# Optimization experiments

Measured on AMD Instinct MI355X. Metric: run time of the kernel, lower is better.

The kernel has to match this reference:

```python
import jax, jax.numpy as jnp
import numpy as np


def _conv2d(x, w, b, padding):
    # x: [N,C,H,W], w: [O,I,kh,kw]
    y = jax.lax.conv_general_dilated(
        x, w, window_strides=(1, 1), padding=padding,
        dimension_numbers=("NCHW", "OIHW", "NCHW"))
    return y + b[None, :, None, None]


def setup_inputs() -> dict:
    key = jax.random.key(0)
    ks = jax.random.split(key, 9)
    s = 0.05
    return {
        "x": jax.random.normal(ks[0], (16, 4, 512, 512), dtype=jnp.float32),
        "w1": jax.random.normal(ks[1], (32, 4, 3, 3), dtype=jnp.float32) * s,
        "b1": jax.random.normal(ks[2], (32,), dtype=jnp.float32) * s,
        "w2": jax.random.normal(ks[3], (4, 32, 3, 3), dtype=jnp.float32) * s,
        "b2": jax.random.normal(ks[4], (4,), dtype=jnp.float32) * s,
        "w_se1": jax.random.normal(ks[5], (16, 32, 1, 1), dtype=jnp.float32) * s,
        "b_se1": jax.random.normal(ks[6], (16,), dtype=jnp.float32) * s,
        "w_se2": jax.random.normal(ks[7], (32, 16, 1, 1), dtype=jnp.float32) * s,
        "b_se2": jax.random.normal(ks[8], (32,), dtype=jnp.float32) * s,
    }


def reference(x, w1, b1, w2, b2, w_se1, b_se1, w_se2, b_se2):
    x1 = x
    # module1: 3x3 conv (4->32) + ReLU
    h = jax.nn.relu(_conv2d(x, w1, b1, padding="SAME"))  # [N,32,H,W]
    se_in = h
    # SE branch: global avg pool -> 1x1 conv -> ReLU -> 1x1 conv -> sigmoid
    p = jnp.mean(h, axis=(2, 3), keepdims=True)  # [N,32,1,1]
    p = jax.nn.relu(_conv2d(p, w_se1, b_se1, padding="VALID"))  # [N,16,1,1]
    p = jax.nn.sigmoid(_conv2d(p, w_se2, b_se2, padding="VALID"))  # [N,32,1,1]
    h = p * se_in  # broadcast channel scaling
    # module2: 3x3 conv (32->4) + ReLU
    h = jax.nn.relu(_conv2d(h, w2, b2, padding="SAME"))  # [N,4,H,W]
    return h * x1  # residual multiply
```

## Files before the change

### kernel.cpp

```cpp
#include <hip/hip_runtime.h>
#include <math.h>

#define IMG 512

typedef __attribute__((ext_vector_type(4))) short short4_t;
typedef __attribute__((ext_vector_type(8))) short short8;
typedef __attribute__((ext_vector_type(4))) float f32x4;
typedef __attribute__((ext_vector_type(16))) float f32x16;
typedef __attribute__((ext_vector_type(2))) unsigned int u32x2;

__device__ __forceinline__ unsigned short f2bf(float f) {
  unsigned u = __builtin_bit_cast(unsigned, f);
  u += 0x7FFFu + ((u >> 16) & 1u);
  return (unsigned short)(u >> 16);
}
__device__ __forceinline__ unsigned cvtpk(float lo, float hi) {
  unsigned r;
  asm("v_cvt_pk_bf16_f32 %0, %1, %2" : "=v"(r) : "v"(lo), "v"(hi));
  return r;
}

__global__ __launch_bounds__(256) void k_prep(const float* __restrict__ w1,
                                              unsigned short* __restrict__ w1f) {
  const int t = threadIdx.x;
  if (t < 192) {
    const int kk = t >> 6, lane = t & 63;
    const int oc = lane & 31, hi = lane >> 5;
#pragma unroll
    for (int j = 0; j < 8; ++j) {
      const int dxp = 2 * hi + (j >> 2), ic = j & 3;
      float v = (dxp < 3) ? w1[((oc * 4 + ic) * 3 + kk) * 3 + dxp] : 0.f;
      w1f[(kk * 64 + lane) * 8 + j] = f2bf(v);
    }
  }
}

__global__ __launch_bounds__(256) void k_pool(
    const float* __restrict__ x, const unsigned short* __restrict__ w1f,
    const float* __restrict__ b1, float* __restrict__ red_out, int use_atomic) {
  __shared__ unsigned short xs[34 * 40 * 4];
  __shared__ float pools[4][2][16];
  const int bid = blockIdx.x;
  const int swz = (bid & 7) * 512 + (bid >> 3);
  const int bx = swz & 15, by = (swz >> 4) & 15, n = swz >> 8;
  const int x0 = bx * 32, y0 = by * 32;
  const int t = threadIdx.x, lane = t & 63, wv = t >> 6;
  const int hi = lane >> 5;

  short8 A1[3];
#pragma unroll
  for (int kk = 0; kk < 3; ++kk)
    A1[kk] = *(const short8*)&w1f[(kk * 64 + lane) * 8];
  float bias_r[16];
#pragma unroll
  for (int r = 0; r < 16; ++r) {
    float bl = b1[(r & 3) + 8 * (r >> 2)], bh = b1[(r & 3) + 8 * (r >> 2) + 4];
    bias_r[r] = hi ? bh : bl;
  }

  const int sx = x0 - 4;
  const long CS = (long)IMG * IMG;
  for (int i = t; i < 340; i += 256) {
    const int row = i / 10, cb = i % 10;
    const int gy = y0 - 1 + row, gx0 = sx + cb * 4;
    f32x4 v0 = {0.f, 0.f, 0.f, 0.f}, v1 = v0, v2 = v0, v3 = v0;
    if (gy >= 0 && gy < IMG && gx0 >= 0 && gx0 < IMG) {
      const float* p = x + (((long)(n * 4) * IMG + gy) * IMG + gx0);
      v0 = *(const f32x4*)p;
      v1 = *(const f32x4*)(p + CS);
      v2 = *(const f32x4*)(p + 2 * CS);
      v3 = *(const f32x4*)(p + 3 * CS);
    }
    unsigned short* d = &xs[(row * 40 + cb * 4) * 4];
#pragma unroll
    for (int j = 0; j < 4; ++j) {
      u32x2 w;
      w[0] = cvtpk(v0[j], v1[j]);
      w[1] = cvtpk(v2[j], v3[j]);
      *(u32x2*)(d + j * 4) = w;
    }
  }
  __syncthreads();

  float pacc[16];
#pragma unroll
  for (int r = 0; r < 16; ++r) pacc[r] = 0.f;
  const int cx0 = (lane & 31) + 2 * hi + 3;
  for (int yy = 0; yy < 8; ++yy) {
    const int rb = wv * 8 + yy;
    const unsigned short* p0 = &xs[(rb * 40 + cx0) * 4];
    f32x16 C;
#pragma unroll
    for (int r = 0; r < 16; ++r) C[r] = bias_r[r];
#define PSTEP(KK)                                                             \
  {                                                                           \
    short4_t bl = *(const short4_t*)(p0 + (KK)*160);                          \
    short4_t bh = *(const short4_t*)(p0 + (KK)*160 + 4);                      \
    short8 B = __builtin_shufflevector(bl, bh, 0, 1, 2, 3, 4, 5, 6, 7);       \
    C = __builtin_amdgcn_mfma_f32_32x32x16_bf16(A1[KK], B, C, 0, 0, 0);       \
  }
    PSTEP(0) PSTEP(1) PSTEP(2)
#undef PSTEP
#pragma unroll
    for (int r = 0; r < 16; ++r) pacc[r] += fmaxf(C[r], 0.f);
  }
#pragma unroll
  for (int r = 0; r < 16; ++r) {
#pragma unroll
    for (int m = 1; m < 32; m <<= 1) pacc[r] += __shfl_xor(pacc[r], m);
  }
  if ((lane & 31) == 0) {
#pragma unroll
    for (int r = 0; r < 16; ++r) pools[wv][hi][r] = pacc[r];
  }
  __syncthreads();
  if (t < 32) {
    const int c = t;
    const int hic = (c >> 2) & 1, reg = (c & 3) + 4 * (c >> 3);
    float s = pools[0][hic][reg] + pools[1][hic][reg] + pools[2][hic][reg] +
              pools[3][hic][reg];
    if (use_atomic) {
      atomicAdd(&red_out[n * 32 + c], s);
    } else {
      red_out[(n * 256 + by * 16 + bx) * 32 + c] = s;
    }
  }
}

__global__ __launch_bounds__(256) void k_se(
    const float* __restrict__ partials, const float* __restrict__ sums,
    const float* __restrict__ w_se1, const float* __restrict__ b_se1,
    const float* __restrict__ w_se2, const float* __restrict__ b_se2,
    const float* __restrict__ w2, unsigned short* __restrict__ w2f, int det) {
  const int n = blockIdx.x, t = threadIdx.x;
  __shared__ float red[8][32];
  __shared__ float mean_s[32], f1[16], p[32];
  if (det) {
    const int c = t & 31, s = t >> 5;
    float a = 0.f;
    for (int i = s * 32; i < s * 32 + 32; ++i)
      a += partials[(n * 256 + i) * 32 + c];
    red[s][c] = a;
    __syncthreads();
    if (t < 32) {
      float v = 0.f;
#pragma unroll
      for (int s2 = 0; s2 < 8; ++s2) v += red[s2][t];
      mean_s[t] = v * (1.0f / (512.f * 512.f));
    }
  } else {
    if (t < 32) mean_s[t] = sums[n * 32 + t] * (1.0f / (512.f * 512.f));
  }
  __syncthreads();
  if (t < 16) {
    float a = b_se1[t];
#pragma unroll
    for (int c = 0; c < 32; ++c) a += w_se1[t * 32 + c] * mean_s[c];
    f1[t] = fmaxf(a, 0.f);
  }
  __syncthreads();
  if (t < 32) {
    float a = b_se2[t];
#pragma unroll
    for (int c = 0; c < 16; ++c) a += w_se2[t * 16 + c] * f1[c];
    p[t] = 1.f / (1.f + expf(-a));
  }
  __syncthreads();
  for (int i = t; i < 9216; i += 256) {
    const int s = i >> 9, rem = i & 511, lane2 = rem >> 3, j = rem & 7;
    const int oc = lane2 & 3, yo = (lane2 >> 2) & 3, cg = lane2 >> 4;
    const int c = cg * 8 + j;
    const int dyy = s / 3, dx = s - dyy * 3, dy = dyy - yo;
    float v = 0.f;
    if (dy >= 0 && dy < 3) v = w2[(oc * 32 + c) * 9 + dy * 3 + dx] * p[c];
    w2f[((n * 18 + s) * 64 + lane2) * 8 + j] = f2bf(v);
  }
}

__global__ __launch_bounds__(256) void k_main(
    const float* __restrict__ x, const unsigned short* __restrict__ w1f,
    const float* __restrict__ b1, const unsigned short* __restrict__ w2f,
    const float* __restrict__ b2, float* __restrict__ out) {
  __shared__ unsigned short xs[20 * 40 * 4];
  __shared__ unsigned short hs[18 * 32 * 32];
  const int bid = blockIdx.x;
  const int swz = (bid & 7) * 1152 + (bid >> 3);
  const int bx = swz % 18;
  const int q = swz / 18;
  const int by = q & 31, n = q >> 5;
  const int x0 = bx * 30, y0 = by * 16;
  const int t = threadIdx.x, lane = t & 63, wv = t >> 6;
  const int hi = lane >> 5;

  short8 A2[18];
#pragma unroll
  for (int s = 0; s < 18; ++s)
    A2[s] = *(const short8*)&w2f[((n * 18 + s) * 64 + lane) * 8];

  short8 A1[3];
#pragma unroll
  for (int kk = 0; kk < 3; ++kk)
    A1[kk] = *(const short8*)&w1f[(kk * 64 + lane) * 8];
  float bias_r[16];
#pragma unroll
  for (int r = 0; r < 16; ++r) {
    float bl = b1[(r & 3) + 8 * (r >> 2)], bh = b1[(r & 3) + 8 * (r >> 2) + 4];
    bias_r[r] = hi ? bh : bl;
  }

  const int sx = (x0 - 4) & ~3;
  const long CS = (long)IMG * IMG;
  for (int i = t; i < 200; i += 256) {
    const int row = i / 10, cb = i % 10;
    const int gy = y0 - 2 + row, gx0 = sx + cb * 4;
    f32x4 v0 = {0.f, 0.f, 0.f, 0.f}, v1 = v0, v2 = v0, v3 = v0;
    if (gy >= 0 && gy < IMG && gx0 >= 0 && gx0 < IMG) {
      const float* p = x + (((long)(n * 4) * IMG + gy) * IMG + gx0);
      v0 = *(const f32x4*)p;
      v1 = *(const f32x4*)(p + CS);
      v2 = *(const f32x4*)(p + 2 * CS);
      v3 = *(const f32x4*)(p + 3 * CS);
    }
    unsigned short* d = &xs[(row * 40 + cb * 4) * 4];
#pragma unroll
    for (int j = 0; j < 4; ++j) {
      u32x2 w;
      w[0] = cvtpk(v0[j], v1[j]);
      w[1] = cvtpk(v2[j], v3[j]);
      *(u32x2*)(d + j * 4) = w;
    }
  }
  __syncthreads();

  {
    const int px = lane & 31;
    const int cx0 = px + 2 * hi + (x0 - 2 - sx);
    const int q2 = (px >> 1) & 3;
    const int gxc = x0 - 1 + px;
    const bool colok = (gxc >= 0) && (gxc < IMG);
    const bool col_int = (x0 >= 1) && (x0 + 30 < IMG);
    for (int hy = wv; hy < 18; hy += 4) {
      const int yi = y0 - 1 + hy;
      const bool row_ok = (yi >= 0) && (yi < IMG);
      const unsigned short* p0 = &xs[(hy * 40 + cx0) * 4];
      f32x16 C;
#pragma unroll
      for (int r = 0; r < 16; ++r) C[r] = bias_r[r];
#define MSTEP(KK)                                                             \
  {                                                                           \
    short4_t bl = *(const short4_t*)(p0 + (KK)*160);                          \
    short4_t bh = *(const short4_t*)(p0 + (KK)*160 + 4);                      \
    short8 B = __builtin_shufflevector(bl, bh, 0, 1, 2, 3, 4, 5, 6, 7);       \
    C = __builtin_amdgcn_mfma_f32_32x32x16_bf16(A1[KK], B, C, 0, 0, 0);       \
  }
      MSTEP(0) MSTEP(1) MSTEP(2)
#undef MSTEP
      const int usb = hy * 1024 + px * 32 + (hi << 2);
      if (row_ok && col_int) {
#pragma unroll
        for (int g = 0; g < 4; ++g) {
          u32x2 w;
          w[0] = cvtpk(fmaxf(C[4 * g + 0], 0.f), fmaxf(C[4 * g + 1], 0.f));
          w[1] = cvtpk(fmaxf(C[4 * g + 2], 0.f), fmaxf(C[4 * g + 3], 0.f));
          *(u32x2*)&hs[usb + ((g ^ q2) << 3)] = w;
        }
      } else if (row_ok) {
#pragma unroll
        for (int g = 0; g < 4; ++g) {
          unsigned p01 = cvtpk(fmaxf(C[4 * g + 0], 0.f), fmaxf(C[4 * g + 1], 0.f));
          unsigned p23 = cvtpk(fmaxf(C[4 * g + 2], 0.f), fmaxf(C[4 * g + 3], 0.f));
          u32x2 w;
          w[0] = colok ? p01 : 0u;
          w[1] = colok ? p23 : 0u;
          *(u32x2*)&hs[usb + ((g ^ q2) << 3)] = w;
        }
      } else {
        u32x2 z;
        z[0] = 0u;
        z[1] = 0u;
#pragma unroll
        for (int g = 0; g < 4; ++g) *(u32x2*)&hs[usb + ((g ^ q2) << 3)] = z;
      }
    }
  }
  __syncthreads();

  {
    const int px16 = lane & 15, cg = lane >> 4;
    const int grp = wv & 1, ybq = wv >> 1;
    const int ox = grp * 16 + px16;
    const int yo = lane >> 4;
    const int gxo = x0 + ox;
    const bool epi_ok = (ox < 30) && (gxo < IMG);
    const float b20 = b2[0], b21 = b2[1], b22 = b2[2], b23 = b2[3];
    const int n4 = n * 4;
    int ph0 = ox + 0, ph1 = ox + 1, ph2 = ox + 2;
    ph2 = ph2 < 31 ? ph2 : 31;
    ph1 = ph1 < 31 ? ph1 : 31;
    const int ba0 = ph0 * 64 + ((cg ^ ((ph0 >> 1) & 3)) << 4);
    const int ba1 = ph1 * 64 + ((cg ^ ((ph1 >> 1) & 3)) << 4);
    const int ba2 = ph2 * 64 + ((cg ^ ((ph2 >> 1) & 3)) << 4);
    const char* hbA = (const char*)hs + (ybq * 8) * 2048;
    const char* hbB = hbA + 4 * 2048;
    f32x4 CA = {0.f, 0.f, 0.f, 0.f}, CB = {0.f, 0.f, 0.f, 0.f};

#define C2(S, DYY, BA)                                                        \
  CA = __builtin_amdgcn_mfma_f32_16x16x32_bf16(                               \
      A2[S], *(const short8*)(hbA + (DYY)*2048 + (BA)), CA, 0, 0, 0);         \
  CB = __builtin_amdgcn_mfma_f32_16x16x32_bf16(                               \
      A2[S], *(const short8*)(hbB + (DYY)*2048 + (BA)), CB, 0, 0, 0);

    C2(0, 0, ba0) C2(1, 0, ba1) C2(2, 0, ba2)
    C2(3, 1, ba0) C2(4, 1, ba1) C2(5, 1, ba2)
    C2(6, 2, ba0) C2(7, 2, ba1) C2(8, 2, ba2)
    C2(9, 3, ba0) C2(10, 3, ba1) C2(11, 3, ba2)
    C2(12, 4, ba0) C2(13, 4, ba1) C2(14, 4, ba2)
    C2(15, 5, ba0) C2(16, 5, ba1) C2(17, 5, ba2)
#undef C2

#define EPI2(CV, YB)                                                          \
  if (epi_ok) {                                                               \
    const int gy = y0 + (YB) + yo;                                            \
    const long i0 = ((long)n4 * IMG + gy) * IMG + gxo;                        \
    out[i0] = fmaxf(CV[0] + b20, 0.f) * x[i0];                                \
    out[i0 + CS] = fmaxf(CV[1] + b21, 0.f) * x[i0 + CS];                      \
    out[i0 + 2 * CS] = fmaxf(CV[2] + b22, 0.f) * x[i0 + 2 * CS];              \
    out[i0 + 3 * CS] = fmaxf(CV[3] + b23, 0.f) * x[i0 + 3 * CS];              \
  }
    EPI2(CA, ybq * 8)
    EPI2(CB, ybq * 8 + 4)
#undef EPI2
  }
}

extern "C" void kernel_launch(void* const* d_in, const int* in_sizes, int n_in,
                              void* d_out, int out_size, void* d_ws,
                              size_t ws_size, hipStream_t stream) {
  const float* x = (const float*)d_in[0];
  const float* w1 = (const float*)d_in[1];
  const float* b1 = (const float*)d_in[2];
  const float* w2 = (const float*)d_in[3];
  const float* b2 = (const float*)d_in[4];
  const float* w_se1 = (const float*)d_in[5];
  const float* b_se1 = (const float*)d_in[6];
  const float* w_se2 = (const float*)d_in[7];
  const float* b_se2 = (const float*)d_in[8];
  float* out = (float*)d_out;
  float* ws = (float*)d_ws;

  float* sums = ws;
  unsigned short* w1f = (unsigned short*)(ws + 512);
  unsigned short* w2f = w1f + 1536;
  float* partials = (float*)(w2f + 147456);
  const size_t need_full =
      512 * 4 + 1536 * 2 + (size_t)147456 * 2 + (size_t)131072 * 4;

  k_prep<<<1, 256, 0, stream>>>(w1, w1f);
  if (ws_size >= need_full) {
    k_pool<<<4096, 256, 0, stream>>>(x, w1f, b1, partials, 0);
    k_se<<<16, 256, 0, stream>>>(partials, sums, w_se1, b_se1, w_se2, b_se2,
                                 w2, w2f, 1);
  } else {
    hipMemsetAsync(sums, 0, 512 * sizeof(float), stream);
    k_pool<<<4096, 256, 0, stream>>>(x, w1f, b1, sums, 1);
    k_se<<<16, 256, 0, stream>>>(partials, sums, w_se1, b_se1, w_se2, b_se2,
                                 w2, w2f, 0);
  }
  k_main<<<9216, 256, 0, stream>>>(x, w1f, b1, w2f, b2, out);
}
```

Baseline: 107.6 us.

## Pipeline conv1 LDS loads, defer w2 weight loads, add occupancy hints and swizzle

Adds a launch-bounds minimum of 3 blocks per SIMD to both main kernels. Fully unrolls the conv1 row loops with a rotating three-register B buffer, so each row reuses two of the previous row's LDS loads. It also rebalances rows across waves (5,5,4,4). The per-image w2 weight fragments are now loaded after conv1 instead of at kernel start, which cuts register pressure during conv1. It also changes the LDS XOR swizzle to reduce bank conflicts, and folds the conv2 bias into the accumulator init.

```diff
diff --git a/kernel.cpp b/kernel.cpp
--- a/kernel.cpp
+++ b/kernel.cpp
@@ -35,7 +35,7 @@
   }
 }
 
-__global__ __launch_bounds__(256) void k_pool(
+__global__ __launch_bounds__(256, 3) void k_pool(
     const float* __restrict__ x, const unsigned short* __restrict__ w1f,
     const float* __restrict__ b1, float* __restrict__ red_out, int use_atomic) {
   __shared__ unsigned short xs[34 * 40 * 4];
@@ -86,24 +86,35 @@
 #pragma unroll
   for (int r = 0; r < 16; ++r) pacc[r] = 0.f;
   const int cx0 = (lane & 31) + 2 * hi + 3;
-  for (int yy = 0; yy < 8; ++yy) {
-    const int rb = wv * 8 + yy;
-    const unsigned short* p0 = &xs[(rb * 40 + cx0) * 4];
-    f32x16 C;
-#pragma unroll
-    for (int r = 0; r < 16; ++r) C[r] = bias_r[r];
-#define PSTEP(KK)                                                             \
+  const unsigned short* pP = &xs[((wv * 8) * 40 + cx0) * 4];
+#define LOADP(K)                                                              \
+  __builtin_shufflevector(*(const short4_t*)(pP + (K)*160),                   \
+                          *(const short4_t*)(pP + (K)*160 + 4), 0, 1, 2, 3,   \
+                          4, 5, 6, 7)
+  short8 Ba, Bb, Bc;
+  Ba = LOADP(0);
+  Bb = LOADP(1);
+#define P_ITER(IT, B0, B1, B2)                                                \
   {                                                                           \
-    short4_t bl = *(const short4_t*)(p0 + (KK)*160);                          \
-    short4_t bh = *(const short4_t*)(p0 + (KK)*160 + 4);                      \
-    short8 B = __builtin_shufflevector(bl, bh, 0, 1, 2, 3, 4, 5, 6, 7);       \
-    C = __builtin_amdgcn_mfma_f32_32x32x16_bf16(A1[KK], B, C, 0, 0, 0);       \
-  }
-    PSTEP(0) PSTEP(1) PSTEP(2)
-#undef PSTEP
-#pragma unroll
-    for (int r = 0; r < 16; ++r) pacc[r] += fmaxf(C[r], 0.f);
-  }
+    B2 = LOADP((IT) + 2);                                                     \
+    f32x16 C;                                                                 \
+    _Pragma("unroll") for (int r = 0; r < 16; ++r) C[r] = bias_r[r];          \
+    C = __builtin_amdgcn_mfma_f32_32x32x16_bf16(A1[0], B0, C, 0, 0, 0);       \
+    C = __builtin_amdgcn_mfma_f32_32x32x16_bf16(A1[1], B1, C, 0, 0, 0);       \
+    C = __builtin_amdgcn_mfma_f32_32x32x16_bf16(A1[2], B2, C, 0, 0, 0);       \
+    _Pragma("unroll") for (int r = 0; r < 16; ++r)                            \
+        pacc[r] += fmaxf(C[r], 0.f);                                          \
+  }
+  P_ITER(0, Ba, Bb, Bc)
+  P_ITER(1, Bb, Bc, Ba)
+  P_ITER(2, Bc, Ba, Bb)
+  P_ITER(3, Ba, Bb, Bc)
+  P_ITER(4, Bb, Bc, Ba)
+  P_ITER(5, Bc, Ba, Bb)
+  P_ITER(6, Ba, Bb, Bc)
+  P_ITER(7, Bb, Bc, Ba)
+#undef P_ITER
+#undef LOADP
 #pragma unroll
   for (int r = 0; r < 16; ++r) {
 #pragma unroll
@@ -177,7 +188,7 @@
   }
 }
 
-__global__ __launch_bounds__(256) void k_main(
+__global__ __launch_bounds__(256, 3) void k_main(
     const float* __restrict__ x, const unsigned short* __restrict__ w1f,
     const float* __restrict__ b1, const unsigned short* __restrict__ w2f,
     const float* __restrict__ b2, float* __restrict__ out) {
@@ -192,11 +203,6 @@
   const int t = threadIdx.x, lane = t & 63, wv = t >> 6;
   const int hi = lane >> 5;
 
-  short8 A2[18];
-#pragma unroll
-  for (int s = 0; s < 18; ++s)
-    A2[s] = *(const short8*)&w2f[((n * 18 + s) * 64 + lane) * 8];
-
   short8 A1[3];
 #pragma unroll
   for (int kk = 0; kk < 3; ++kk)
@@ -235,54 +241,89 @@
   {
     const int px = lane & 31;
     const int cx0 = px + 2 * hi + (x0 - 2 - sx);
-    const int q2 = (px >> 1) & 3;
+    const int q2 = ((px >> 1) ^ (px >> 3)) & 3;
     const int gxc = x0 - 1 + px;
     const bool colok = (gxc >= 0) && (gxc < IMG);
     const bool col_int = (x0 >= 1) && (x0 + 30 < IMG);
-    for (int hy = wv; hy < 18; hy += 4) {
-      const int yi = y0 - 1 + hy;
-      const bool row_ok = (yi >= 0) && (yi < IMG);
-      const unsigned short* p0 = &xs[(hy * 40 + cx0) * 4];
-      f32x16 C;
-#pragma unroll
-      for (int r = 0; r < 16; ++r) C[r] = bias_r[r];
-#define MSTEP(KK)                                                             \
+    const int R0 = (wv < 2) ? wv * 5 : 10 + (wv - 2) * 4;
+    const unsigned short* pR = &xs[(R0 * 40 + cx0) * 4];
+#define LOADX(K)                                                              \
+  __builtin_shufflevector(*(const short4_t*)(pR + (K)*160),                   \
+                          *(const short4_t*)(pR + (K)*160 + 4), 0, 1, 2, 3,   \
+                          4, 5, 6, 7)
+    short8 Ba, Bb, Bc;
+    Ba = LOADX(0);
+    Bb = LOADX(1);
+#define C1_ITER(IT, B0, B1, B2)                                               \
   {                                                                           \
-    short4_t bl = *(const short4_t*)(p0 + (KK)*160);                          \
-    short4_t bh = *(const short4_t*)(p0 + (KK)*160 + 4);                      \
-    short8 B = __builtin_shufflevector(bl, bh, 0, 1, 2, 3, 4, 5, 6, 7);       \
-    C = __builtin_amdgcn_mfma_f32_32x32x16_bf16(A1[KK], B, C, 0, 0, 0);       \
-  }
-      MSTEP(0) MSTEP(1) MSTEP(2)
-#undef MSTEP
-      const int usb = hy * 1024 + px * 32 + (hi << 2);
-      if (row_ok && col_int) {
-#pragma unroll
-        for (int g = 0; g < 4; ++g) {
-          u32x2 w;
-          w[0] = cvtpk(fmaxf(C[4 * g + 0], 0.f), fmaxf(C[4 * g + 1], 0.f));
-          w[1] = cvtpk(fmaxf(C[4 * g + 2], 0.f), fmaxf(C[4 * g + 3], 0.f));
-          *(u32x2*)&hs[usb + ((g ^ q2) << 3)] = w;
-        }
-      } else if (row_ok) {
-#pragma unroll
-        for (int g = 0; g < 4; ++g) {
-          unsigned p01 = cvtpk(fmaxf(C[4 * g + 0], 0.f), fmaxf(C[4 * g + 1], 0.f));
-          unsigned p23 = cvtpk(fmaxf(C[4 * g + 2], 0.f), fmaxf(C[4 * g + 3], 0.f));
-          u32x2 w;
-          w[0] = colok ? p01 : 0u;
-          w[1] = colok ? p23 : 0u;
-          *(u32x2*)&hs[usb + ((g ^ q2) << 3)] = w;
-        }
-      } else {
-        u32x2 z;
-        z[0] = 0u;
-        z[1] = 0u;
-#pragma unroll
-        for (int g = 0; g < 4; ++g) *(u32x2*)&hs[usb + ((g ^ q2) << 3)] = z;
-      }
-    }
-  }
+    B2 = LOADX((IT) + 2);                                                     \
+    const int hy = R0 + (IT);                                                 \
+    const int yi = y0 - 1 + hy;                                               \
+    const bool row_ok = (yi >= 0) && (yi < IMG);                              \
+    f32x16 C;                                                                 \
+    _Pragma("unroll") for (int r = 0; r < 16; ++r) C[r] = bias_r[r];          \
+    C = __builtin_amdgcn_mfma_f32_32x32x16_bf16(A1[0], B0, C, 0, 0, 0);       \
+    C = __builtin_amdgcn_mfma_f32_32x32x16_bf16(A1[1], B1, C, 0, 0, 0);       \
+    C = __builtin_amdgcn_mfma_f32_32x32x16_bf16(A1[2], B2, C, 0, 0, 0);       \
+    const int usb = hy * 1024 + px * 32 + (hi << 2);                          \
+    if (row_ok && col_int) {                                                  \
+      _Pragma("unroll") for (int g = 0; g < 4; ++g) {                         \
+        u32x2 w;                                                              \
+        w[0] = cvtpk(fmaxf(C[4 * g + 0], 0.f), fmaxf(C[4 * g + 1], 0.f));     \
+        w[1] = cvtpk(fmaxf(C[4 * g + 2], 0.f), fmaxf(C[4 * g + 3], 0.f));     \
+        *(u32x2*)&hs[usb + ((g ^ q2) << 3)] = w;                              \
+      }                                                                       \
+    } else if (row_ok) {                                                      \
+      _Pragma("unroll") for (int g = 0; g < 4; ++g) {                         \
+        unsigned p01 =                                                        \
+            cvtpk(fmaxf(C[4 * g + 0], 0.f), fmaxf(C[4 * g + 1], 0.f));        \
+        unsigned p23 =                                                        \
+            cvtpk(fmaxf(C[4 * g + 2], 0.f), fmaxf(C[4 * g + 3], 0.f));        \
+        u32x2 w;                                                              \
+        w[0] = colok ? p01 : 0u;                                              \
+        w[1] = colok ? p23 : 0u;                                              \
+        *(u32x2*)&hs[usb + ((g ^ q2) << 3)] = w;                              \
+      }                                                                       \
+    } else {                                                                  \
+      u32x2 z;                                                                \
+      z[0] = 0u;                                                              \
+      z[1] = 0u;                                                              \
+      _Pragma("unroll") for (int g = 0; g < 4; ++g)                           \
+          *(u32x2*)&hs[usb + ((g ^ q2) << 3)] = z;                            \
+    }                                                                         \
+  }
+    C1_ITER(0, Ba, Bb, Bc)
+    C1_ITER(1, Bb, Bc, Ba)
+    C1_ITER(2, Bc, Ba, Bb)
+    C1_ITER(3, Ba, Bb, Bc)
+    if (wv < 2) C1_ITER(4, Bb, Bc, Ba)
+#undef C1_ITER
+#undef LOADX
+  }
+
+  const unsigned short* w2b = w2f + (size_t)n * 9216 + lane * 8;
+  short8 A2_0 = *(const short8*)(w2b + 0 * 512);
+  short8 A2_1 = *(const short8*)(w2b + 1 * 512);
+  short8 A2_2 = *(const short8*)(w2b + 2 * 512);
+  short8 A2_3 = *(const short8*)(w2b + 3 * 512);
+  short8 A2_4 = *(const short8*)(w2b + 4 * 512);
+  short8 A2_5 = *(const short8*)(w2b + 5 * 512);
+  short8 A2_6 = *(const short8*)(w2b + 6 * 512);
+  short8 A2_7 = *(const short8*)(w2b + 7 * 512);
+  short8 A2_8 = *(const short8*)(w2b + 8 * 512);
+  short8 A2_9 = *(const short8*)(w2b + 9 * 512);
+  short8 A2_10 = *(const short8*)(w2b + 10 * 512);
+  short8 A2_11 = *(const short8*)(w2b + 11 * 512);
+  short8 A2_12 = *(const short8*)(w2b + 12 * 512);
+  short8 A2_13 = *(const short8*)(w2b + 13 * 512);
+  short8 A2_14 = *(const short8*)(w2b + 14 * 512);
+  short8 A2_15 = *(const short8*)(w2b + 15 * 512);
+  short8 A2_16 = *(const short8*)(w2b + 16 * 512);
+  short8 A2_17 = *(const short8*)(w2b + 17 * 512);
+  asm volatile("" ::"v"(A2_0), "v"(A2_1), "v"(A2_2), "v"(A2_3), "v"(A2_4),
+               "v"(A2_5), "v"(A2_6), "v"(A2_7), "v"(A2_8), "v"(A2_9),
+               "v"(A2_10), "v"(A2_11), "v"(A2_12), "v"(A2_13), "v"(A2_14),
+               "v"(A2_15), "v"(A2_16), "v"(A2_17));
   __syncthreads();
 
   {
@@ -297,18 +338,19 @@
     int ph0 = ox + 0, ph1 = ox + 1, ph2 = ox + 2;
     ph2 = ph2 < 31 ? ph2 : 31;
     ph1 = ph1 < 31 ? ph1 : 31;
-    const int ba0 = ph0 * 64 + ((cg ^ ((ph0 >> 1) & 3)) << 4);
-    const int ba1 = ph1 * 64 + ((cg ^ ((ph1 >> 1) & 3)) << 4);
-    const int ba2 = ph2 * 64 + ((cg ^ ((ph2 >> 1) & 3)) << 4);
+    const int ba0 = ph0 * 64 + ((cg ^ (((ph0 >> 1) ^ (ph0 >> 3)) & 3)) << 4);
+    const int ba1 = ph1 * 64 + ((cg ^ (((ph1 >> 1) ^ (ph1 >> 3)) & 3)) << 4);
+    const int ba2 = ph2 * 64 + ((cg ^ (((ph2 >> 1) ^ (ph2 >> 3)) & 3)) << 4);
     const char* hbA = (const char*)hs + (ybq * 8) * 2048;
     const char* hbB = hbA + 4 * 2048;
-    f32x4 CA = {0.f, 0.f, 0.f, 0.f}, CB = {0.f, 0.f, 0.f, 0.f};
+    f32x4 CA = {b20, b21, b22, b23};
+    f32x4 CB = {b20, b21, b22, b23};
 
 #define C2(S, DYY, BA)                                                        \
   CA = __builtin_amdgcn_mfma_f32_16x16x32_bf16(                               \
-      A2[S], *(const short8*)(hbA + (DYY)*2048 + (BA)), CA, 0, 0, 0);         \
+      A2_##S, *(const short8*)(hbA + (DYY)*2048 + (BA)), CA, 0, 0, 0);        \
   CB = __builtin_amdgcn_mfma_f32_16x16x32_bf16(                               \
-      A2[S], *(const short8*)(hbB + (DYY)*2048 + (BA)), CB, 0, 0, 0);
+      A2_##S, *(const short8*)(hbB + (DYY)*2048 + (BA)), CB, 0, 0, 0);
 
     C2(0, 0, ba0) C2(1, 0, ba1) C2(2, 0, ba2)
     C2(3, 1, ba0) C2(4, 1, ba1) C2(5, 1, ba2)
@@ -322,10 +364,10 @@
   if (epi_ok) {                                                               \
     const int gy = y0 + (YB) + yo;                                            \
     const long i0 = ((long)n4 * IMG + gy) * IMG + gxo;                        \
-    out[i0] = fmaxf(CV[0] + b20, 0.f) * x[i0];                                \
-    out[i0 + CS] = fmaxf(CV[1] + b21, 0.f) * x[i0 + CS];                      \
-    out[i0 + 2 * CS] = fmaxf(CV[2] + b22, 0.f) * x[i0 + 2 * CS];              \
-    out[i0 + 3 * CS] = fmaxf(CV[3] + b23, 0.f) * x[i0 + 3 * CS];              \
+    out[i0] = fmaxf(CV[0], 0.f) * x[i0];                                      \
+    out[i0 + CS] = fmaxf(CV[1], 0.f) * x[i0 + CS];                            \
+    out[i0 + 2 * CS] = fmaxf(CV[2], 0.f) * x[i0 + 2 * CS];                    \
+    out[i0 + 3 * CS] = fmaxf(CV[3], 0.f) * x[i0 + 3 * CS];                    \
   }
     EPI2(CA, ybq * 8)
     EPI2(CB, ybq * 8 + 4)
```

New measurement: 105.5 us. Within noise of the previous version (-1.9%).
